# Kernel tuning notes

Hardware: AMD Instinct MI355X
Metric: run time of the kernel (lower is better)

Reference implementation:

```python
import jax, jax.numpy as jnp
import numpy as np

B, C_IN, T = 4, 256, 8192
LAYERS, STACKS = 24, 4
RES, GATE, SKIP, K = 128, 256, 128, 3
LPS = LAYERS // STACKS  # layers per stack -> dilation = 2**(i % LPS)
SQRT_HALF = 0.7071067811865476


def setup_inputs() -> dict:
    key = jax.random.key(0)
    ks = jax.random.split(key, 14)
    s = 0.08  # small init so the 24-layer stack stays well-scaled
    inp = {
        "x": jax.random.normal(ks[0], (B, C_IN, T), jnp.float32),
        "first_w": jax.random.normal(ks[1], (RES, C_IN), jnp.float32) * s,
        "first_b": jnp.zeros((RES,), jnp.float32),
        "conv_w": jax.random.normal(ks[2], (LAYERS, GATE, RES, K), jnp.float32) * s,
        "conv_b": jnp.zeros((LAYERS, GATE), jnp.float32),
        "out_w": jax.random.normal(ks[3], (LAYERS, RES, GATE // 2), jnp.float32) * s,
        "out_b": jnp.zeros((LAYERS, RES), jnp.float32),
        "skip_w": jax.random.normal(ks[4], (LAYERS, SKIP, GATE // 2), jnp.float32) * s,
        "skip_b": jnp.zeros((LAYERS, SKIP), jnp.float32),
        "last1_w": jax.random.normal(ks[5], (SKIP, SKIP), jnp.float32) * s,
        "last1_b": jnp.zeros((SKIP,), jnp.float32),
        "last2_w": jax.random.normal(ks[6], (C_IN, SKIP), jnp.float32) * s,
        "last2_b": jnp.zeros((C_IN,), jnp.float32),
    }
    return inp


def _conv1x1(w, b, h):
    # h: [B, C, T], w: [O, C]
    return jnp.einsum('oc,bct->bot', w, h) + b[None, :, None]


def _causal_dilated_conv(h, w, b, dilation):
    # left pad == torch symmetric pad (k-1)*d followed by crop to first T (causal)
    pad = (K - 1) * dilation
    hp = jnp.pad(h, ((0, 0), (0, 0), (pad, 0)))
    y = jax.lax.conv_general_dilated(
        hp, w, window_strides=(1,), padding='VALID',
        rhs_dilation=(dilation,), dimension_numbers=('NCH', 'OIH', 'NCH'))
    return y + b[None, :, None]


def reference(x, first_w, first_b, conv_w, conv_b, out_w, out_b,
              skip_w, skip_b, last1_w, last1_b, last2_w, last2_b):
    h = _conv1x1(first_w, first_b, x)  # [B, RES, T]
    skips = jnp.zeros((x.shape[0], SKIP, x.shape[-1]), h.dtype)
    for i in range(LAYERS):
        d = 2 ** (i % LPS)
        y = _causal_dilated_conv(h, conv_w[i], conv_b[i], d)  # [B, GATE, T]
        a, g = jnp.split(y, 2, axis=1)
        z = jnp.tanh(a) * jax.nn.sigmoid(g)  # gated tanh*sigmoid
        skips = skips + _conv1x1(skip_w[i], skip_b[i], z)
        h = (_conv1x1(out_w[i], out_b[i], z) + h) * SQRT_HALF  # residual
    skips = skips * (1.0 / LAYERS) ** 0.5
    out = jax.nn.relu(skips)
    out = jax.nn.relu(_conv1x1(last1_w, last1_b, out))
    out = _conv1x1(last2_w, last2_b, out)  # logits [B, 256, T]
    return out
```

## Files before the change

### kernel.cpp

```cpp
#include <hip/hip_runtime.h>

#define B 4
#define CIN 256
#define T 8192
#define NL 24
#define TP (64 + T + 8)
#define TT 128
#define SQRT_HALF 0.70710678118654752f
#define SKIP_SCALE 0.20412414523193150f

typedef unsigned short u16;
typedef __attribute__((ext_vector_type(4))) float f32x4;
typedef __attribute__((ext_vector_type(8))) short s16x8;
typedef __attribute__((ext_vector_type(4))) short s16x4;

__device__ inline u16 f2bf(float f) {
  unsigned u = __float_as_uint(f);
  return (u16)((u + 0x7fffu + ((u >> 16) & 1u)) >> 16);
}

__device__ inline void gload_lds16(const void* g, void* l) {
  __builtin_amdgcn_global_load_lds(
      (const __attribute__((address_space(1))) unsigned*)g,
      (__attribute__((address_space(3))) unsigned*)l, 16, 0, 0);
}

__device__ inline float gate_fn(float a, float g) {
  float af = fminf(fabsf(a), 20.f);
  float E = __expf(2.f * af);
  float F = __expf(-g);
  float z = (E - 1.f) / ((E + 1.f) * (1.f + F));
  return copysignf(z, a);
}

__global__ void cvt_convw(const float* __restrict__ src, u16* __restrict__ dst) {
  int i = blockIdx.x * 256 + threadIdx.x;
  if (i >= NL * 3 * 256 * 128) return;
  int c = i & 127, o = (i >> 7) & 255, kk = (i >> 15) % 3, l = (i >> 15) / 3;
  dst[i] = f2bf(src[(((size_t)l * 256 + o) * 128 + c) * 3 + kk]);
}
__global__ void cvt_sow(const float* __restrict__ skw, const float* __restrict__ otw,
                        u16* __restrict__ dst) {
  int i = blockIdx.x * 256 + threadIdx.x;
  if (i >= NL * 256 * 128) return;
  int c = i & 127, r = (i >> 7) & 255, l = i >> 15;
  float v = (r < 128) ? skw[((size_t)l * 128 + r) * 128 + c]
                      : otw[((size_t)l * 128 + (r - 128)) * 128 + c];
  dst[i] = f2bf(v);
}
__global__ void cvt_plain(const float* __restrict__ s, u16* __restrict__ d, int n) {
  int i = blockIdx.x * 256 + threadIdx.x;
  if (i < n) d[i] = f2bf(s[i]);
}
__global__ void padzero(u16* __restrict__ hb) {
  int i = blockIdx.x * 256 + threadIdx.x;
  if (i >= B * 64 * 128) return;
  int c = i & 127, r = (i >> 7) & 63, b = i >> 13;
  hb[((size_t)b * TP + r) * 128 + c] = 0;
}

__global__ __launch_bounds__(256, 2)
void first_kernel(const float* __restrict__ x, const u16* __restrict__ wf,
                  const float* __restrict__ fb, float* __restrict__ hf,
                  u16* __restrict__ hb) {
  __shared__ u16 xT[64 * 256];
  __shared__ u16 hoT[64 * 128];
  const int tid = threadIdx.x, wv = tid >> 6, lane = tid & 63, lo = lane & 15, hi = lane >> 4;
  const int t0 = blockIdx.x * 64, b = blockIdx.y;

  for (int it = 0; it < 16; it++) {
    int idx = tid + it * 256;
    int c = idx >> 4, t4 = (idx & 15) << 2;
    f32x4 v = *(const f32x4*)(x + ((size_t)b * CIN + c) * T + t0 + t4);
    #pragma unroll
    for (int i = 0; i < 4; i++) {
      int t = t4 + i;
      *(u16*)((char*)xT + t * 512 + ((c * 2) ^ ((t & 7) << 4))) = f2bf(v[i]);
    }
  }
  __syncthreads();

  f32x4 acc[2][4];
  #pragma unroll
  for (int m = 0; m < 2; m++)
    #pragma unroll
    for (int n = 0; n < 4; n++) acc[m][n] = (f32x4){0.f, 0.f, 0.f, 0.f};

  for (int s = 0; s < 8; s++) {
    s16x8 af[2], bf[4];
    #pragma unroll
    for (int m = 0; m < 2; m++)
      af[m] = *(const s16x8*)(wf + (size_t)(wv * 32 + m * 16 + lo) * CIN + s * 32 + hi * 8);
    #pragma unroll
    for (int n = 0; n < 4; n++) {
      int t = n * 16 + lo;
      bf[n] = *(const s16x8*)((const char*)xT + t * 512 + ((s * 64 + hi * 16) ^ ((t & 7) << 4)));
    }
    #pragma unroll
    for (int m = 0; m < 2; m++)
      #pragma unroll
      for (int n = 0; n < 4; n++)
        acc[m][n] = __builtin_amdgcn_mfma_f32_16x16x32_bf16(af[m], bf[n], acc[m][n], 0, 0, 0);
  }

  #pragma unroll
  for (int m = 0; m < 2; m++) {
    int c0 = wv * 32 + m * 16 + hi * 4;
    f32x4 bv = *(const f32x4*)(fb + c0);
    #pragma unroll
    for (int n = 0; n < 4; n++) {
      int t = n * 16 + lo;
      f32x4 h = acc[m][n] + bv;
      *(f32x4*)(hf + ((size_t)b * T + t0 + t) * 128 + c0) = h;
      s16x4 pk;
      #pragma unroll
      for (int j = 0; j < 4; j++) pk[j] = (short)f2bf(h[j]);
      *(s16x4*)((char*)hoT + t * 256 + ((c0 * 2) ^ ((t & 7) << 4))) = pk;
    }
  }
  __syncthreads();
  u16* gd = hb + ((size_t)b * TP + 64 + t0) * 128;
  for (int i = tid; i < 1024; i += 256)
    *(s16x8*)((char*)gd + i * 16) = *(const s16x8*)((const char*)hoT + i * 16);
}

__global__ __launch_bounds__(512, 2)
void layer_kernel(const u16* __restrict__ hbin, u16* __restrict__ hbout,
                  float* __restrict__ hf, float* __restrict__ skip,
                  const u16* __restrict__ wcv, const float* __restrict__ cb,
                  const u16* __restrict__ wso, const float* __restrict__ sb,
                  const float* __restrict__ ob, int d, int first) {
  __shared__ u16 h_s[196 * 128];
  __shared__ u16 zh[128 * 128];
  const int tid = threadIdx.x, wv = tid >> 6, lane = tid & 63, lo = lane & 15, hi = lane >> 4;
  const int t0 = blockIdx.x * TT, b = blockIdx.y;
  const int R = TT + 2 * d;
  const int nch = (R * 256 + 1023) >> 10;

  const char* src = (const char*)(hbin + ((size_t)b * TP + (64 + t0 - 2 * d)) * 128);
  for (int ch = wv; ch < nch; ch += 8)
    gload_lds16(src + ch * 1024 + lane * 16, (char*)h_s + ch * 1024);
  __syncthreads();

  f32x4 acc[2][8];
  #pragma unroll
  for (int m = 0; m < 2; m++)
    #pragma unroll
    for (int n = 0; n < 8; n++) acc[m][n] = (f32x4){0.f, 0.f, 0.f, 0.f};
  const int oa = wv * 16, og = 128 + wv * 16;

  for (int k = 0; k < 3; k++) {
    const int jb = k * d;
    const int st = ((lo + (k + 6) * d) & 7) << 4;
    for (int s = 0; s < 4; s++) {
      s16x8 af0 = *(const s16x8*)(wcv + ((size_t)(k * 256 + oa + lo)) * 128 + s * 32 + hi * 8);
      s16x8 af1 = *(const s16x8*)(wcv + ((size_t)(k * 256 + og + lo)) * 128 + s * 32 + hi * 8);
      const int cbyte = s * 64 + hi * 16;
      s16x8 bf[8];
      #pragma unroll
      for (int n = 0; n < 8; n++) {
        int j = n * 16 + lo + jb;
        bf[n] = *(const s16x8*)((const char*)h_s + j * 256 + (cbyte ^ st));
      }
      #pragma unroll
      for (int n = 0; n < 8; n++) {
        acc[0][n] = __builtin_amdgcn_mfma_f32_16x16x32_bf16(af0, bf[n], acc[0][n], 0, 0, 0);
        acc[1][n] = __builtin_amdgcn_mfma_f32_16x16x32_bf16(af1, bf[n], acc[1][n], 0, 0, 0);
      }
    }
  }

  f32x4 ba = *(const f32x4*)(cb + oa + hi * 4);
  f32x4 bg = *(const f32x4*)(cb + og + hi * 4);
  #pragma unroll
  for (int n = 0; n < 8; n++) {
    int t = n * 16 + lo;
    s16x4 pk;
    #pragma unroll
    for (int j = 0; j < 4; j++)
      pk[j] = (short)f2bf(gate_fn(acc[0][n][j] + ba[j], acc[1][n][j] + bg[j]));
    *(s16x4*)((char*)zh + t * 256 + (((oa + hi * 4) * 2) ^ ((t & 7) << 4))) = pk;
  }
  __syncthreads();

  f32x4 ac2[2][8];
  #pragma unroll
  for (int m = 0; m < 2; m++)
    #pragma unroll
    for (int n = 0; n < 8; n++) ac2[m][n] = (f32x4){0.f, 0.f, 0.f, 0.f};
  const int ro = wv * 32;
  for (int s = 0; s < 4; s++) {
    s16x8 af0 = *(const s16x8*)(wso + (size_t)(ro + lo) * 128 + s * 32 + hi * 8);
    s16x8 af1 = *(const s16x8*)(wso + (size_t)(ro + 16 + lo) * 128 + s * 32 + hi * 8);
    const int cbyte = s * 64 + hi * 16;
    s16x8 bf[8];
    #pragma unroll
    for (int n = 0; n < 8; n++) {
      int t = n * 16 + lo;
      bf[n] = *(const s16x8*)((const char*)zh + t * 256 + (cbyte ^ ((t & 7) << 4)));
    }
    #pragma unroll
    for (int n = 0; n < 8; n++) {
      ac2[0][n] = __builtin_amdgcn_mfma_f32_16x16x32_bf16(af0, bf[n], ac2[0][n], 0, 0, 0);
      ac2[1][n] = __builtin_amdgcn_mfma_f32_16x16x32_bf16(af1, bf[n], ac2[1][n], 0, 0, 0);
    }
  }
  __syncthreads();

  if (wv < 4) {
    #pragma unroll
    for (int m = 0; m < 2; m++) {
      int c0 = wv * 32 + m * 16 + hi * 4;
      f32x4 sb4 = *(const f32x4*)(sb + c0);
      #pragma unroll
      for (int n = 0; n < 8; n++) {
        size_t off = ((size_t)b * T + t0 + n * 16 + lo) * 128 + c0;
        f32x4 r = ac2[m][n] + sb4;
        if (!first) r += *(const f32x4*)(skip + off);
        *(f32x4*)(skip + off) = r;
      }
    }
  } else {
    #pragma unroll
    for (int m = 0; m < 2; m++) {
      int c0 = (wv - 4) * 32 + m * 16 + hi * 4;
      f32x4 ob4 = *(const f32x4*)(ob + c0);
      #pragma unroll
      for (int n = 0; n < 8; n++) {
        int tl = n * 16 + lo;
        size_t off = ((size_t)b * T + t0 + tl) * 128 + c0;
        f32x4 hn = (ac2[m][n] + ob4 + *(const f32x4*)(hf + off)) * SQRT_HALF;
        *(f32x4*)(hf + off) = hn;
        s16x4 pk;
        #pragma unroll
        for (int j = 0; j < 4; j++) pk[j] = (short)f2bf(hn[j]);
        *(s16x4*)((char*)zh + tl * 256 + ((c0 * 2) ^ ((tl & 7) << 4))) = pk;
      }
    }
  }
  __syncthreads();
  u16* gd = hbout + ((size_t)b * TP + 64 + t0) * 128;
  for (int i = tid; i < 2048; i += 512)
    *(s16x8*)((char*)gd + i * 16) = *(const s16x8*)((const char*)zh + i * 16);
}

__global__ __launch_bounds__(256, 2)
void head1_kernel(const float* __restrict__ skip, const u16* __restrict__ w1,
                  const float* __restrict__ b1, u16* __restrict__ s1) {
  __shared__ u16 sT[64 * 128];
  const int tid = threadIdx.x, wv = tid >> 6, lane = tid & 63, lo = lane & 15, hi = lane >> 4;
  const int t0 = blockIdx.x * 64, b = blockIdx.y;

  for (int it = 0; it < 8; it++) {
    int idx = tid + it * 256;
    int t = idx >> 5, c4 = idx & 31;
    f32x4 v = *(const f32x4*)(skip + ((size_t)b * T + t0 + t) * 128 + c4 * 4);
    s16x4 pk;
    #pragma unroll
    for (int i = 0; i < 4; i++) pk[i] = (short)f2bf(fmaxf(v[i] * SKIP_SCALE, 0.f));
    *(s16x4*)((char*)sT + t * 256 + ((c4 * 8) ^ ((t & 7) << 4))) = pk;
  }
  __syncthreads();

  f32x4 acc[2][4];
  #pragma unroll
  for (int m = 0; m < 2; m++)
    #pragma unroll
    for (int n = 0; n < 4; n++) acc[m][n] = (f32x4){0.f, 0.f, 0.f, 0.f};
  for (int s = 0; s < 4; s++) {
    s16x8 af[2], bf[4];
    #pragma unroll
    for (int m = 0; m < 2; m++)
      af[m] = *(const s16x8*)(w1 + (size_t)(wv * 32 + m * 16 + lo) * 128 + s * 32 + hi * 8);
    #pragma unroll
    for (int n = 0; n < 4; n++) {
      int t = n * 16 + lo;
      bf[n] = *(const s16x8*)((const char*)sT + t * 256 + ((s * 64 + hi * 16) ^ ((t & 7) << 4)));
    }
    #pragma unroll
    for (int m = 0; m < 2; m++)
      #pragma unroll
      for (int n = 0; n < 4; n++)
        acc[m][n] = __builtin_amdgcn_mfma_f32_16x16x32_bf16(af[m], bf[n], acc[m][n], 0, 0, 0);
  }
  #pragma unroll
  for (int m = 0; m < 2; m++) {
    int c0 = wv * 32 + m * 16 + hi * 4;
    f32x4 bv = *(const f32x4*)(b1 + c0);
    #pragma unroll
    for (int n = 0; n < 4; n++) {
      int t = n * 16 + lo;
      s16x4 pk;
      #pragma unroll
      for (int j = 0; j < 4; j++) pk[j] = (short)f2bf(fmaxf(acc[m][n][j] + bv[j], 0.f));
      *(s16x4*)((char*)s1 + ((size_t)b * T + t0 + t) * 256 + ((c0 * 2) ^ ((t & 7) << 4))) = pk;
    }
  }
}

__global__ __launch_bounds__(256, 2)
void head2_kernel(const u16* __restrict__ s1, const u16* __restrict__ w2,
                  const float* __restrict__ b2, float* __restrict__ out) {
  __shared__ u16 s1T[64 * 128];
  const int tid = threadIdx.x, wv = tid >> 6, lane = tid & 63, lo = lane & 15, hi = lane >> 4;
  const int t0 = blockIdx.x * 64, b = blockIdx.y;

  const char* src = (const char*)(s1 + ((size_t)b * T + t0) * 128);
  for (int ch = wv; ch < 16; ch += 4)
    gload_lds16(src + ch * 1024 + lane * 16, (char*)s1T + ch * 1024);
  __syncthreads();

  f32x4 acc[4][4];
  #pragma unroll
  for (int m = 0; m < 4; m++)
    #pragma unroll
    for (int n = 0; n < 4; n++) acc[m][n] = (f32x4){0.f, 0.f, 0.f, 0.f};
  for (int s = 0; s < 4; s++) {
    s16x8 af[4], bf[4];
    #pragma unroll
    for (int m = 0; m < 4; m++)
      af[m] = *(const s16x8*)(w2 + (size_t)(wv * 64 + m * 16 + lo) * 128 + s * 32 + hi * 8);
    #pragma unroll
    for (int n = 0; n < 4; n++) {
      int t = n * 16 + lo;
      bf[n] = *(const s16x8*)((const char*)s1T + t * 256 + ((s * 64 + hi * 16) ^ ((t & 7) << 4)));
    }
    #pragma unroll
    for (int m = 0; m < 4; m++)
      #pragma unroll
      for (int n = 0; n < 4; n++)
        acc[m][n] = __builtin_amdgcn_mfma_f32_16x16x32_bf16(af[m], bf[n], acc[m][n], 0, 0, 0);
  }
  #pragma unroll
  for (int m = 0; m < 4; m++) {
    int c0 = wv * 64 + m * 16 + hi * 4;
    f32x4 bv = *(const f32x4*)(b2 + c0);
    #pragma unroll
    for (int n = 0; n < 4; n++) {
      int t = t0 + n * 16 + lo;
      f32x4 r = acc[m][n] + bv;
      #pragma unroll
      for (int j = 0; j < 4; j++) out[((size_t)b * CIN + c0 + j) * T + t] = r[j];
    }
  }
}

extern "C" void kernel_launch(void* const* d_in, const int* in_sizes, int n_in,
                              void* d_out, int out_size, void* d_ws, size_t ws_size,
                              hipStream_t stream) {
  const float* x       = (const float*)d_in[0];
  const float* first_w = (const float*)d_in[1];
  const float* first_b = (const float*)d_in[2];
  const float* conv_w  = (const float*)d_in[3];
  const float* conv_b  = (const float*)d_in[4];
  const float* out_w   = (const float*)d_in[5];
  const float* out_b   = (const float*)d_in[6];
  const float* skip_w  = (const float*)d_in[7];
  const float* skip_b  = (const float*)d_in[8];
  const float* last1_w = (const float*)d_in[9];
  const float* last1_b = (const float*)d_in[10];
  const float* last2_w = (const float*)d_in[11];
  const float* last2_b = (const float*)d_in[12];
  float* out = (float*)d_out;

  u16* wsp  = (u16*)d_ws;
  u16* wcv  = wsp;
  u16* wsoB = wcv + (size_t)NL * 3 * 256 * 128;
  u16* wfB  = wsoB + (size_t)NL * 256 * 128;
  u16* w1B  = wfB + 128 * 256;
  u16* w2B  = w1B + 128 * 128;
  u16* hb0  = w2B + 256 * 128;
  u16* hb1  = hb0 + (size_t)B * TP * 128;
  u16* s1   = hb0;

  float* hf   = (float*)d_out;
  float* skip = hf + (size_t)B * T * 128;

  cvt_convw<<<NL * 3 * 256 * 128 / 256, 256, 0, stream>>>(conv_w, wcv);
  cvt_sow<<<NL * 256 * 128 / 256, 256, 0, stream>>>(skip_w, out_w, wsoB);
  cvt_plain<<<128, 256, 0, stream>>>(first_w, wfB, 128 * 256);
  cvt_plain<<<64, 256, 0, stream>>>(last1_w, w1B, 128 * 128);
  cvt_plain<<<128, 256, 0, stream>>>(last2_w, w2B, 256 * 128);
  padzero<<<128, 256, 0, stream>>>(hb0);
  padzero<<<128, 256, 0, stream>>>(hb1);

  dim3 g64(T / 64, B), g128(T / TT, B);
  first_kernel<<<g64, 256, 0, stream>>>(x, wfB, first_b, hf, hb0);
  for (int i = 0; i < NL; i++) {
    int d = 1 << (i % 6);
    layer_kernel<<<g128, 512, 0, stream>>>(
        (i & 1) ? hb1 : hb0, (i & 1) ? hb0 : hb1, hf, skip,
        wcv + (size_t)i * 3 * 256 * 128, conv_b + (size_t)i * 256,
        wsoB + (size_t)i * 256 * 128, skip_b + (size_t)i * 128,
        out_b + (size_t)i * 128, d, i == 0 ? 1 : 0);
  }
  head1_kernel<<<g64, 256, 0, stream>>>(skip, w1B, last1_b, s1);
  head2_kernel<<<g64, 256, 0, stream>>>(s1, w2B, last2_b, out);
}
```

Before: 829.0 us.

## Halve layer time tile, raise occupancy, reuse accumulators, cheaper gate math

Reduces the layer kernel time tile from 128 to 64, shrinking shared memory and accumulator registers so launch bounds can request 4 blocks per CU and the grid doubles. Reuses the conv accumulator array for the second GEMM, fully unrolls many loops, and rewrites the tanh*sigmoid gate using hardware reciprocal. This is meant to improve latency hiding and cut transcendental cost. In exchange the halo reload fraction grows (2d rows per 64 instead of per 128), weights are reloaded by twice as many blocks, and rcp approximation slightly changes numerics.

```diff
diff --git a/kernel.cpp b/kernel.cpp
--- a/kernel.cpp
+++ b/kernel.cpp
@@ -5,7 +5,7 @@
 #define T 8192
 #define NL 24
 #define TP (64 + T + 8)
-#define TT 128
+#define TT 64
 #define SQRT_HALF 0.70710678118654752f
 #define SKIP_SCALE 0.20412414523193150f
 
@@ -26,11 +26,10 @@
 }
 
 __device__ inline float gate_fn(float a, float g) {
-  float af = fminf(fabsf(a), 20.f);
-  float E = __expf(2.f * af);
-  float F = __expf(-g);
-  float z = (E - 1.f) / ((E + 1.f) * (1.f + F));
-  return copysignf(z, a);
+  float e2 = __expf(-2.f * fabsf(a));
+  float th = (1.f - e2) * __builtin_amdgcn_rcpf(1.f + e2);
+  float sg = __builtin_amdgcn_rcpf(1.f + __expf(-g));
+  return copysignf(th, a) * sg;
 }
 
 __global__ void cvt_convw(const float* __restrict__ src, u16* __restrict__ dst) {
@@ -68,6 +67,7 @@
   const int tid = threadIdx.x, wv = tid >> 6, lane = tid & 63, lo = lane & 15, hi = lane >> 4;
   const int t0 = blockIdx.x * 64, b = blockIdx.y;
 
+  #pragma unroll
   for (int it = 0; it < 16; it++) {
     int idx = tid + it * 256;
     int c = idx >> 4, t4 = (idx & 15) << 2;
@@ -86,6 +86,7 @@
     #pragma unroll
     for (int n = 0; n < 4; n++) acc[m][n] = (f32x4){0.f, 0.f, 0.f, 0.f};
 
+  #pragma unroll
   for (int s = 0; s < 8; s++) {
     s16x8 af[2], bf[4];
     #pragma unroll
@@ -120,18 +121,19 @@
   }
   __syncthreads();
   u16* gd = hb + ((size_t)b * TP + 64 + t0) * 128;
-  for (int i = tid; i < 1024; i += 256)
-    *(s16x8*)((char*)gd + i * 16) = *(const s16x8*)((const char*)hoT + i * 16);
-}
-
-__global__ __launch_bounds__(512, 2)
+  #pragma unroll
+  for (int i = 0; i < 4; i++)
+    *(s16x8*)((char*)gd + (tid + i * 256) * 16) = *(const s16x8*)((const char*)hoT + (tid + i * 256) * 16);
+}
+
+__global__ __launch_bounds__(512, 4)
 void layer_kernel(const u16* __restrict__ hbin, u16* __restrict__ hbout,
                   float* __restrict__ hf, float* __restrict__ skip,
                   const u16* __restrict__ wcv, const float* __restrict__ cb,
                   const u16* __restrict__ wso, const float* __restrict__ sb,
                   const float* __restrict__ ob, int d, int first) {
-  __shared__ u16 h_s[196 * 128];
-  __shared__ u16 zh[128 * 128];
+  __shared__ u16 h_s[128 * 128];
+  __shared__ u16 zh[64 * 128];
   const int tid = threadIdx.x, wv = tid >> 6, lane = tid & 63, lo = lane & 15, hi = lane >> 4;
   const int t0 = blockIdx.x * TT, b = blockIdx.y;
   const int R = TT + 2 * d;
@@ -142,67 +144,71 @@
     gload_lds16(src + ch * 1024 + lane * 16, (char*)h_s + ch * 1024);
   __syncthreads();
 
-  f32x4 acc[2][8];
+  f32x4 acc[2][4];
   #pragma unroll
   for (int m = 0; m < 2; m++)
     #pragma unroll
-    for (int n = 0; n < 8; n++) acc[m][n] = (f32x4){0.f, 0.f, 0.f, 0.f};
+    for (int n = 0; n < 4; n++) acc[m][n] = (f32x4){0.f, 0.f, 0.f, 0.f};
   const int oa = wv * 16, og = 128 + wv * 16;
 
+  #pragma unroll
   for (int k = 0; k < 3; k++) {
     const int jb = k * d;
     const int st = ((lo + (k + 6) * d) & 7) << 4;
+    #pragma unroll
     for (int s = 0; s < 4; s++) {
       s16x8 af0 = *(const s16x8*)(wcv + ((size_t)(k * 256 + oa + lo)) * 128 + s * 32 + hi * 8);
       s16x8 af1 = *(const s16x8*)(wcv + ((size_t)(k * 256 + og + lo)) * 128 + s * 32 + hi * 8);
       const int cbyte = s * 64 + hi * 16;
-      s16x8 bf[8];
-      #pragma unroll
-      for (int n = 0; n < 8; n++) {
+      s16x8 bf[4];
+      #pragma unroll
+      for (int n = 0; n < 4; n++) {
         int j = n * 16 + lo + jb;
         bf[n] = *(const s16x8*)((const char*)h_s + j * 256 + (cbyte ^ st));
       }
       #pragma unroll
-      for (int n = 0; n < 8; n++) {
+      for (int n = 0; n < 4; n++) {
         acc[0][n] = __builtin_amdgcn_mfma_f32_16x16x32_bf16(af0, bf[n], acc[0][n], 0, 0, 0);
         acc[1][n] = __builtin_amdgcn_mfma_f32_16x16x32_bf16(af1, bf[n], acc[1][n], 0, 0, 0);
       }
     }
   }
 
-  f32x4 ba = *(const f32x4*)(cb + oa + hi * 4);
-  f32x4 bg = *(const f32x4*)(cb + og + hi * 4);
-  #pragma unroll
-  for (int n = 0; n < 8; n++) {
-    int t = n * 16 + lo;
-    s16x4 pk;
-    #pragma unroll
-    for (int j = 0; j < 4; j++)
-      pk[j] = (short)f2bf(gate_fn(acc[0][n][j] + ba[j], acc[1][n][j] + bg[j]));
-    *(s16x4*)((char*)zh + t * 256 + (((oa + hi * 4) * 2) ^ ((t & 7) << 4))) = pk;
-  }
-  __syncthreads();
-
-  f32x4 ac2[2][8];
+  {
+    f32x4 ba = *(const f32x4*)(cb + oa + hi * 4);
+    f32x4 bg = *(const f32x4*)(cb + og + hi * 4);
+    #pragma unroll
+    for (int n = 0; n < 4; n++) {
+      int t = n * 16 + lo;
+      s16x4 pk;
+      #pragma unroll
+      for (int j = 0; j < 4; j++)
+        pk[j] = (short)f2bf(gate_fn(acc[0][n][j] + ba[j], acc[1][n][j] + bg[j]));
+      *(s16x4*)((char*)zh + t * 256 + (((oa + hi * 4) * 2) ^ ((t & 7) << 4))) = pk;
+    }
+  }
+  __syncthreads();
+
   #pragma unroll
   for (int m = 0; m < 2; m++)
     #pragma unroll
-    for (int n = 0; n < 8; n++) ac2[m][n] = (f32x4){0.f, 0.f, 0.f, 0.f};
+    for (int n = 0; n < 4; n++) acc[m][n] = (f32x4){0.f, 0.f, 0.f, 0.f};
   const int ro = wv * 32;
+  #pragma unroll
   for (int s = 0; s < 4; s++) {
     s16x8 af0 = *(const s16x8*)(wso + (size_t)(ro + lo) * 128 + s * 32 + hi * 8);
     s16x8 af1 = *(const s16x8*)(wso + (size_t)(ro + 16 + lo) * 128 + s * 32 + hi * 8);
     const int cbyte = s * 64 + hi * 16;
-    s16x8 bf[8];
-    #pragma unroll
-    for (int n = 0; n < 8; n++) {
+    s16x8 bf[4];
+    #pragma unroll
+    for (int n = 0; n < 4; n++) {
       int t = n * 16 + lo;
       bf[n] = *(const s16x8*)((const char*)zh + t * 256 + (cbyte ^ ((t & 7) << 4)));
     }
     #pragma unroll
-    for (int n = 0; n < 8; n++) {
-      ac2[0][n] = __builtin_amdgcn_mfma_f32_16x16x32_bf16(af0, bf[n], ac2[0][n], 0, 0, 0);
-      ac2[1][n] = __builtin_amdgcn_mfma_f32_16x16x32_bf16(af1, bf[n], ac2[1][n], 0, 0, 0);
+    for (int n = 0; n < 4; n++) {
+      acc[0][n] = __builtin_amdgcn_mfma_f32_16x16x32_bf16(af0, bf[n], acc[0][n], 0, 0, 0);
+      acc[1][n] = __builtin_amdgcn_mfma_f32_16x16x32_bf16(af1, bf[n], acc[1][n], 0, 0, 0);
     }
   }
   __syncthreads();
@@ -213,9 +219,9 @@
       int c0 = wv * 32 + m * 16 + hi * 4;
       f32x4 sb4 = *(const f32x4*)(sb + c0);
       #pragma unroll
-      for (int n = 0; n < 8; n++) {
+      for (int n = 0; n < 4; n++) {
         size_t off = ((size_t)b * T + t0 + n * 16 + lo) * 128 + c0;
-        f32x4 r = ac2[m][n] + sb4;
+        f32x4 r = acc[m][n] + sb4;
         if (!first) r += *(const f32x4*)(skip + off);
         *(f32x4*)(skip + off) = r;
       }
@@ -226,10 +232,10 @@
       int c0 = (wv - 4) * 32 + m * 16 + hi * 4;
       f32x4 ob4 = *(const f32x4*)(ob + c0);
       #pragma unroll
-      for (int n = 0; n < 8; n++) {
+      for (int n = 0; n < 4; n++) {
         int tl = n * 16 + lo;
         size_t off = ((size_t)b * T + t0 + tl) * 128 + c0;
-        f32x4 hn = (ac2[m][n] + ob4 + *(const f32x4*)(hf + off)) * SQRT_HALF;
+        f32x4 hn = (acc[m][n] + ob4 + *(const f32x4*)(hf + off)) * SQRT_HALF;
         *(f32x4*)(hf + off) = hn;
         s16x4 pk;
         #pragma unroll
@@ -240,8 +246,9 @@
   }
   __syncthreads();
   u16* gd = hbout + ((size_t)b * TP + 64 + t0) * 128;
-  for (int i = tid; i < 2048; i += 512)
-    *(s16x8*)((char*)gd + i * 16) = *(const s16x8*)((const char*)zh + i * 16);
+  #pragma unroll
+  for (int i = 0; i < 2; i++)
+    *(s16x8*)((char*)gd + (tid + i * 512) * 16) = *(const s16x8*)((const char*)zh + (tid + i * 512) * 16);
 }
 
 __global__ __launch_bounds__(256, 2)
@@ -251,6 +258,7 @@
   const int tid = threadIdx.x, wv = tid >> 6, lane = tid & 63, lo = lane & 15, hi = lane >> 4;
   const int t0 = blockIdx.x * 64, b = blockIdx.y;
 
+  #pragma unroll
   for (int it = 0; it < 8; it++) {
     int idx = tid + it * 256;
     int t = idx >> 5, c4 = idx & 31;
@@ -267,6 +275,7 @@
   for (int m = 0; m < 2; m++)
     #pragma unroll
     for (int n = 0; n < 4; n++) acc[m][n] = (f32x4){0.f, 0.f, 0.f, 0.f};
+  #pragma unroll
   for (int s = 0; s < 4; s++) {
     s16x8 af[2], bf[4];
     #pragma unroll
@@ -306,8 +315,9 @@
   const int t0 = blockIdx.x * 64, b = blockIdx.y;
 
   const char* src = (const char*)(s1 + ((size_t)b * T + t0) * 128);
-  for (int ch = wv; ch < 16; ch += 4)
-    gload_lds16(src + ch * 1024 + lane * 16, (char*)s1T + ch * 1024);
+  #pragma unroll
+  for (int i = 0; i < 4; i++)
+    gload_lds16(src + (wv + i * 4) * 1024 + lane * 16, (char*)s1T + (wv + i * 4) * 1024);
   __syncthreads();
 
   f32x4 acc[4][4];
@@ -315,6 +325,7 @@
   for (int m = 0; m < 4; m++)
     #pragma unroll
     for (int n = 0; n < 4; n++) acc[m][n] = (f32x4){0.f, 0.f, 0.f, 0.f};
+  #pragma unroll
   for (int s = 0; s < 4; s++) {
     s16x8 af[4], bf[4];
     #pragma unroll
@@ -384,11 +395,11 @@
   padzero<<<128, 256, 0, stream>>>(hb0);
   padzero<<<128, 256, 0, stream>>>(hb1);
 
-  dim3 g64(T / 64, B), g128(T / TT, B);
+  dim3 g64(T / 64, B), gL(T / TT, B);
   first_kernel<<<g64, 256, 0, stream>>>(x, wfB, first_b, hf, hb0);
   for (int i = 0; i < NL; i++) {
     int d = 1 << (i % 6);
-    layer_kernel<<<g128, 512, 0, stream>>>(
+    layer_kernel<<<gL, 512, 0, stream>>>(
         (i & 1) ? hb1 : hb0, (i & 1) ? hb0 : hb1, hf, skip,
         wcv + (size_t)i * 3 * 256 * 128, conv_b + (size_t)i * 256,
         wsoB + (size_t)i * 256 * 128, skip_b + (size_t)i * 128,
```

New measurement: 759.2 us. 8.4% less time.
